# Kernel tuning notes

Hardware: AMD Instinct MI355X
Metric: run time of the kernel (lower is better)

## Reference

```python
import jax, jax.numpy as jnp
import numpy as np

DIM = 1536
HEADS = 12
HD = DIM // HEADS           # 128
C = HD // 2                 # 64 rotary pairs per head
B = 1
F_, H_, W_ = 16, 16, 16
S = F_ * H_ * W_            # 4096
MAXPOS = 1024
EPS = 1e-6
SPLITS = (C - 2 * (C // 3), C // 3, C // 3)  # (22, 21, 21)


def setup_inputs() -> dict:
    key = jax.random.key(0)
    ks = jax.random.split(key, 8)
    std = 0.02
    x = jax.random.normal(ks[0], (B, S, DIM), jnp.float32)
    seq_lens = jnp.full((B,), S, dtype=jnp.int32)
    grid_sizes = jnp.tile(jnp.array([[F_, H_, W_]], jnp.int32), (B, 1))
    # rotary angle table: per split, theta_j = pos / 10000^(j/size)
    angs = []
    pos = jnp.arange(MAXPOS, dtype=jnp.float32)
    for sz in SPLITS:
        inv = 1.0 / (10000.0 ** (jnp.arange(sz, dtype=jnp.float32) / sz))
        angs.append(jnp.outer(pos, inv))
    freqs = jnp.concatenate(angs, axis=1)  # [MAXPOS, C]
    return {
        "x": x,
        "seq_lens": seq_lens,
        "grid_sizes": grid_sizes,
        "freqs": freqs,
        "wq": jax.random.normal(ks[1], (DIM, DIM), jnp.float32) * std,
        "bq": jnp.zeros((DIM,), jnp.float32),
        "wk": jax.random.normal(ks[2], (DIM, DIM), jnp.float32) * std,
        "bk": jnp.zeros((DIM,), jnp.float32),
        "wv": jax.random.normal(ks[3], (DIM, DIM), jnp.float32) * std,
        "bv": jnp.zeros((DIM,), jnp.float32),
        "wo": jax.random.normal(ks[4], (DIM, DIM), jnp.float32) * std,
        "bo": jnp.zeros((DIM,), jnp.float32),
        "gq": jnp.ones((DIM,), jnp.float32),
        "gk": jnp.ones((DIM,), jnp.float32),
    }


def _rms_norm(x, g):
    # x * rsqrt(mean(x^2) + eps) * g  (WanRMSNorm)
    var = jnp.mean(jnp.square(x), axis=-1, keepdims=True)
    return x * jax.lax.rsqrt(var + EPS) * g


def _rope(x, freqs, f, h, w):
    # x: [b, s, n, hd]; freqs: [MAXPOS, C] angles; grid (f,h,w), s = f*h*w
    fa = freqs[:f, : SPLITS[0]]
    ha = freqs[:h, SPLITS[0] : SPLITS[0] + SPLITS[1]]
    wa = freqs[:w, SPLITS[0] + SPLITS[1] :]
    ang = jnp.concatenate(
        [
            jnp.broadcast_to(fa[:, None, None, :], (f, h, w, SPLITS[0])),
            jnp.broadcast_to(ha[None, :, None, :], (f, h, w, SPLITS[1])),
            jnp.broadcast_to(wa[None, None, :, :], (f, h, w, SPLITS[2])),
        ],
        axis=-1,
    ).reshape(f * h * w, 1, C)  # [s, 1, C] broadcasts over heads
    cos, sin = jnp.cos(ang), jnp.sin(ang)
    xr = x[..., 0::2]  # real parts of complex pairs
    xi = x[..., 1::2]  # imag parts
    out_r = xr * cos - xi * sin
    out_i = xr * sin + xi * cos
    return jnp.stack([out_r, out_i], axis=-1).reshape(x.shape)


def reference(x, seq_lens, grid_sizes, freqs, wq, bq, wk, bk, wv, bv, wo, bo, gq, gk):
    b, s = x.shape[:2]
    q = _rms_norm(x @ wq.T + bq, gq).reshape(b, s, HEADS, HD)
    k = _rms_norm(x @ wk.T + bk, gk).reshape(b, s, HEADS, HD)
    v = (x @ wv.T + bv).reshape(b, s, HEADS, HD)
    # all samples share the same grid (static for jit)
    q = _rope(q, freqs, F_, H_, W_)
    k = _rope(k, freqs, F_, H_, W_)
    scale = 1.0 / np.sqrt(HD)
    scores = jnp.einsum("bqnd,bknd->bnqk", q, k) * scale  # [b, n, s, s]
    k_pos = jnp.arange(s)
    mask = k_pos[None, None, None, :] < seq_lens[:, None, None, None]
    scores = scores + jnp.where(mask, 0.0, -1e9)
    attn = jax.nn.softmax(scores, axis=-1)
    out = jnp.einsum("bnqk,bknd->bqnd", attn, v).reshape(b, s, DIM)
    return out @ wo.T + bo
```

## Files before the change

kernel.cpp:

```cpp
#include <hip/hip_runtime.h>
#include <hip/hip_bf16.h>

#define DIM   1536
#define HEADS 12
#define HD    128
#define SEQ   4096
#define QSCALE 0.08838834764831845f
#define LOG2E 1.44269504088896f

typedef __attribute__((ext_vector_type(8))) short short8;
typedef __attribute__((ext_vector_type(4))) float f32x4;
typedef __attribute__((ext_vector_type(16))) float f32x16;

__device__ __forceinline__ unsigned short f2bf(float f) {
    __hip_bfloat16 h = __float2bfloat16(f);
    return *reinterpret_cast<unsigned short*>(&h);
}
__device__ __forceinline__ float bf2f(unsigned short u) {
    return __uint_as_float(((unsigned int)u) << 16);
}
__device__ __forceinline__ void async_cp16(void* lds, const void* g) {
    __builtin_amdgcn_global_load_lds(
        (const __attribute__((address_space(1))) unsigned int*)g,
        (__attribute__((address_space(3))) unsigned int*)lds, 16, 0, 0);
}

__global__ __launch_bounds__(256) void gemm_qkv(
    const float* __restrict__ x,
    const float* __restrict__ wq, const float* __restrict__ bq,
    const float* __restrict__ wk, const float* __restrict__ bk,
    const float* __restrict__ wv, const float* __restrict__ bv,
    __hip_bfloat16* __restrict__ yq, __hip_bfloat16* __restrict__ yk,
    __hip_bfloat16* __restrict__ vrow)
{
    __shared__ __align__(16) short As[128][40];
    __shared__ __align__(16) short Bs[128][40];
    const int z  = blockIdx.z;
    const float* W    = (z == 0) ? wq : (z == 1) ? wk : wv;
    const float* bias = (z == 0) ? bq : (z == 1) ? bk : bv;
    __hip_bfloat16* outp = (z == 0) ? yq : (z == 1) ? yk : vrow;
    const int bm0 = blockIdx.x * 128;
    const int bn0 = blockIdx.y * 128;
    const int tid  = threadIdx.x;
    const int lane = tid & 63;
    const int wid  = tid >> 6;
    const int wm = (wid >> 1) * 64;
    const int wn = (wid & 1)  * 64;
    const int fr = lane & 15;
    const int fc = (lane >> 4) * 8;
    const int srow = tid >> 3;
    const int scol = (tid & 7) * 4;

    f32x4 acc[4][4] = {};

    for (int kt = 0; kt < DIM; kt += 32) {
        #pragma unroll
        for (int p = 0; p < 4; ++p) {
            const int r = srow + p * 32;
            float4 va = *reinterpret_cast<const float4*>(&x[(size_t)(bm0 + r) * DIM + kt + scol]);
            float4 vb = *reinterpret_cast<const float4*>(&W[(size_t)(bn0 + r) * DIM + kt + scol]);
            uint2 pa, pb;
            pa.x = (unsigned int)f2bf(va.x) | ((unsigned int)f2bf(va.y) << 16);
            pa.y = (unsigned int)f2bf(va.z) | ((unsigned int)f2bf(va.w) << 16);
            pb.x = (unsigned int)f2bf(vb.x) | ((unsigned int)f2bf(vb.y) << 16);
            pb.y = (unsigned int)f2bf(vb.z) | ((unsigned int)f2bf(vb.w) << 16);
            *reinterpret_cast<uint2*>(&As[r][scol]) = pa;
            *reinterpret_cast<uint2*>(&Bs[r][scol]) = pb;
        }
        __syncthreads();
        short8 af[4], bf8[4];
        #pragma unroll
        for (int m = 0; m < 4; m++) af[m]  = *reinterpret_cast<const short8*>(&As[wm + m * 16 + fr][fc]);
        #pragma unroll
        for (int n = 0; n < 4; n++) bf8[n] = *reinterpret_cast<const short8*>(&Bs[wn + n * 16 + fr][fc]);
        #pragma unroll
        for (int m = 0; m < 4; m++)
            #pragma unroll
            for (int n = 0; n < 4; n++)
                acc[m][n] = __builtin_amdgcn_mfma_f32_16x16x32_bf16(af[m], bf8[n], acc[m][n], 0, 0, 0);
        __syncthreads();
    }

    const int crow0 = bm0 + wm + (lane >> 4) * 4;
    const int ccol0 = bn0 + wn + fr;
    #pragma unroll
    for (int n = 0; n < 4; n++) {
        const int col = ccol0 + n * 16;
        const float bb = bias[col];
        #pragma unroll
        for (int m = 0; m < 4; m++)
            #pragma unroll
            for (int r = 0; r < 4; r++)
                outp[(size_t)(crow0 + m * 16 + r) * DIM + col] =
                    __float2bfloat16(acc[m][n][r] + bb);
    }
}

__global__ __launch_bounds__(256) void rmsnorm_rope(
    __hip_bfloat16* __restrict__ yq, __hip_bfloat16* __restrict__ yk,
    const float* __restrict__ gq, const float* __restrict__ gk,
    const float* __restrict__ freqs)
{
    const int s = blockIdx.x;
    const int z = blockIdx.y;
    __hip_bfloat16* y = z ? yk : yq;
    const float* g = z ? gk : gq;
    const int t = threadIdx.x;

    float xr[3], xi[3];
    float ss = 0.f;
    #pragma unroll
    for (int i = 0; i < 3; i++) {
        const int p = t + i * 256;
        const unsigned int uu = *reinterpret_cast<const unsigned int*>(&y[(size_t)s * DIM + 2 * p]);
        xr[i] = bf2f((unsigned short)(uu & 0xffffu));
        xi[i] = bf2f((unsigned short)(uu >> 16));
        ss += xr[i] * xr[i] + xi[i] * xi[i];
    }
    #pragma unroll
    for (int m = 1; m < 64; m <<= 1) ss += __shfl_xor(ss, m, 64);
    __shared__ float red[4];
    if ((t & 63) == 0) red[t >> 6] = ss;
    __syncthreads();
    const float sum = red[0] + red[1] + red[2] + red[3];
    const float rs = rsqrtf(sum * (1.0f / DIM) + 1e-6f);
    const int f = s >> 8, hh = (s >> 4) & 15, ww = s & 15;
    const float osc = z ? 1.0f : QSCALE;
    #pragma unroll
    for (int i = 0; i < 3; i++) {
        const int p = t + i * 256;
        const int cc = p & 63;
        const int pos = (cc < 22) ? f : (cc < 43) ? hh : ww;
        const float ang = freqs[pos * 64 + cc];
        float sn, cs;
        sincosf(ang, &sn, &cs);
        const float a = xr[i] * rs * g[2 * p];
        const float b = xi[i] * rs * g[2 * p + 1];
        const unsigned int pk = (unsigned int)f2bf((a * cs - b * sn) * osc)
                              | ((unsigned int)f2bf((a * sn + b * cs) * osc) << 16);
        *reinterpret_cast<unsigned int*>(&y[(size_t)s * DIM + 2 * p]) = pk;
    }
}

__global__ __launch_bounds__(256) void transpose_v(
    const __hip_bfloat16* __restrict__ vrow,
    __hip_bfloat16* __restrict__ vT)
{
    __shared__ __align__(16) short tile[64][72];
    const int s0 = blockIdx.x * 64;
    const int c0 = blockIdx.y * 64;
    const int t = threadIdx.x;
    #pragma unroll
    for (int i = 0; i < 2; i++) {
        const int ch = t + i * 256;
        const int r = ch >> 3, cc = (ch & 7) * 8;
        *reinterpret_cast<int4*>(&tile[r][cc]) =
            *reinterpret_cast<const int4*>(&vrow[(size_t)(s0 + r) * DIM + c0 + cc]);
    }
    __syncthreads();
    #pragma unroll
    for (int i = 0; i < 2; i++) {
        const int ch = t + i * 256;
        const int c = ch & 63, sc = (ch >> 6) * 8;
        unsigned int w0 = (unsigned short)tile[sc + 0][c] | ((unsigned int)(unsigned short)tile[sc + 1][c] << 16);
        unsigned int w1 = (unsigned short)tile[sc + 2][c] | ((unsigned int)(unsigned short)tile[sc + 3][c] << 16);
        unsigned int w2 = (unsigned short)tile[sc + 4][c] | ((unsigned int)(unsigned short)tile[sc + 5][c] << 16);
        unsigned int w3 = (unsigned short)tile[sc + 6][c] | ((unsigned int)(unsigned short)tile[sc + 7][c] << 16);
        int4 val;
        val.x = (int)w0; val.y = (int)w1; val.z = (int)w2; val.w = (int)w3;
        *reinterpret_cast<int4*>(&vT[(size_t)(c0 + c) * SEQ + s0 + sc]) = val;
    }
}

__global__ __launch_bounds__(256, 2) void flash_attn(
    const __hip_bfloat16* __restrict__ qb,
    const __hip_bfloat16* __restrict__ kb,
    const __hip_bfloat16* __restrict__ vT,
    const int* __restrict__ seq_lens,
    __hip_bfloat16* __restrict__ attno)
{
    __shared__ __align__(16) short Ks[2][64][128];
    __shared__ __align__(16) short Vs[2][128][64];
    const int qt = blockIdx.x;
    const int h  = blockIdx.y;
    const int tid = threadIdx.x;
    const int lane = tid & 63;
    const int w = tid >> 6;
    const int q5 = lane & 31;
    const int hi = lane >> 5;
    const int seqlen = seq_lens[0];
    const int swz = (lane & 7) << 4;

    short8 qf[8];
    const int qrow = qt * 128 + w * 32 + q5;
    #pragma unroll
    for (int s = 0; s < 8; s++)
        qf[s] = *reinterpret_cast<const short8*>(&qb[(size_t)qrow * DIM + h * HD + s * 16 + hi * 8]);

    f32x16 oacc[4] = {};
    float m = -1e30f, l = 0.f;

    const int kROW = w * 4 + (lane >> 4);
    const int kCOL = ((lane & 15) ^ (kROW & 7)) * 8;
    const int vROW = w * 8 + (lane >> 3);
    const int vCOL = (((lane & 7) ^ (vROW & 7))) * 8;

    #pragma unroll
    for (int i = 0; i < 4; i++) {
        async_cp16(&Ks[0][i * 16 + w * 4][0],
                   kb + (size_t)(i * 16 + kROW) * DIM + h * HD + kCOL);
        async_cp16(&Vs[0][i * 32 + w * 8][0],
                   vT + ((size_t)h * HD + i * 32 + vROW) * SEQ + vCOL);
    }
    __syncthreads();

    for (int t = 0; t < SEQ / 64; t++) {
        const int cur = t & 1;
        const int kbase = t * 64;
        if (t + 1 < SEQ / 64) {
            const int nb = kbase + 64;
            #pragma unroll
            for (int i = 0; i < 4; i++) {
                async_cp16(&Ks[cur ^ 1][i * 16 + w * 4][0],
                           kb + (size_t)(nb + i * 16 + kROW) * DIM + h * HD + kCOL);
                async_cp16(&Vs[cur ^ 1][i * 32 + w * 8][0],
                           vT + ((size_t)h * HD + i * 32 + vROW) * SEQ + nb + vCOL);
            }
        }
        const char* Kp = (const char*)&Ks[cur][0][0];
        const char* Vp = (const char*)&Vs[cur][0][0];

        f32x16 sacc[2] = {};
        __builtin_amdgcn_s_setprio(1);
        #pragma unroll
        for (int s = 0; s < 8; s++) {
            #pragma unroll
            for (int kbk = 0; kbk < 2; kbk++) {
                short8 kf = *reinterpret_cast<const short8*>(
                    Kp + (kbk * 32 + q5) * 256 + ((s * 32 + hi * 16) ^ swz));
                sacc[kbk] = __builtin_amdgcn_mfma_f32_32x32x16_bf16(kf, qf[s], sacc[kbk], 0, 0, 0);
            }
        }
        __builtin_amdgcn_s_setprio(0);

        float tmax = -1e30f;
        if (kbase + 64 <= seqlen) {
            #pragma unroll
            for (int kbk = 0; kbk < 2; kbk++)
                #pragma unroll
                for (int r = 0; r < 16; r++) tmax = fmaxf(tmax, sacc[kbk][r]);
        } else {
            #pragma unroll
            for (int kbk = 0; kbk < 2; kbk++) {
                #pragma unroll
                for (int r = 0; r < 16; r++) {
                    const int key = kbase + kbk * 32 + (r & 3) + 8 * (r >> 2) + 4 * hi;
                    const float sv = (key < seqlen) ? sacc[kbk][r] : -1e30f;
                    sacc[kbk][r] = sv;
                    tmax = fmaxf(tmax, sv);
                }
            }
        }
        tmax = fmaxf(tmax, __shfl_xor(tmax, 32, 64));

        if (!__all(tmax <= m + 8.0f)) {
            const float mn = fmaxf(m, tmax);
            const float alpha = exp2f((m - mn) * LOG2E);
            m = mn;
            l *= alpha;
            #pragma unroll
            for (int cb = 0; cb < 4; cb++)
                #pragma unroll
                for (int r = 0; r < 16; r++) oacc[cb][r] *= alpha;
        }

        float ps = 0.f;
        #pragma unroll
        for (int kbk = 0; kbk < 2; kbk++) {
            #pragma unroll
            for (int r = 0; r < 16; r++) {
                const float p = exp2f((sacc[kbk][r] - m) * LOG2E);
                sacc[kbk][r] = p;
                ps += p;
            }
        }
        ps += __shfl_xor(ps, 32, 64);
        l += ps;

        unsigned int W[2][4][2];
        #pragma unroll
        for (int kbk = 0; kbk < 2; kbk++)
            #pragma unroll
            for (int tq = 0; tq < 4; tq++) {
                W[kbk][tq][0] = (unsigned int)f2bf(sacc[kbk][4 * tq + 0])
                              | ((unsigned int)f2bf(sacc[kbk][4 * tq + 1]) << 16);
                W[kbk][tq][1] = (unsigned int)f2bf(sacc[kbk][4 * tq + 2])
                              | ((unsigned int)f2bf(sacc[kbk][4 * tq + 3]) << 16);
            }

        #pragma unroll
        for (int ks = 0; ks < 4; ks++) {
            const int kbk = ks >> 1;
            const int te = (ks & 1) * 2, to = te + 1;
            const int a0 = (int)W[kbk][te][0], a1 = (int)W[kbk][te][1];
            const int b0 = (int)W[kbk][to][0], b1 = (int)W[kbk][to][1];
            const int xa0 = __shfl_xor(a0, 32, 64);
            const int xa1 = __shfl_xor(a1, 32, 64);
            const int xb0 = __shfl_xor(b0, 32, 64);
            const int xb1 = __shfl_xor(b1, 32, 64);
            int4 pwv;
            pwv.x = hi ? xb0 : a0;
            pwv.y = hi ? xb1 : a1;
            pwv.z = hi ? b0  : xa0;
            pwv.w = hi ? b1  : xa1;
            const short8 pf = __builtin_bit_cast(short8, pwv);
            __builtin_amdgcn_s_setprio(1);
            #pragma unroll
            for (int cb = 0; cb < 4; cb++) {
                short8 vf = *reinterpret_cast<const short8*>(
                    Vp + (cb * 32 + q5) * 128 + ((ks * 32 + hi * 16) ^ swz));
                oacc[cb] = __builtin_amdgcn_mfma_f32_32x32x16_bf16(vf, pf, oacc[cb], 0, 0, 0);
            }
            __builtin_amdgcn_s_setprio(0);
        }
        __syncthreads();
    }

    const float inv_l = 1.f / l;
    const size_t obase = (size_t)qrow * DIM + h * HD;
    #pragma unroll
    for (int cb = 0; cb < 4; cb++) {
        #pragma unroll
        for (int tq = 0; tq < 4; tq++) {
            uint2 pko;
            pko.x = (unsigned int)f2bf(oacc[cb][4 * tq + 0] * inv_l)
                  | ((unsigned int)f2bf(oacc[cb][4 * tq + 1] * inv_l) << 16);
            pko.y = (unsigned int)f2bf(oacc[cb][4 * tq + 2] * inv_l)
                  | ((unsigned int)f2bf(oacc[cb][4 * tq + 3] * inv_l) << 16);
            *reinterpret_cast<uint2*>(&attno[obase + cb * 32 + 8 * tq + 4 * hi]) = pko;
        }
    }
}

__global__ __launch_bounds__(256) void gemm_out(
    const __hip_bfloat16* __restrict__ A,
    const float* __restrict__ W,
    const float* __restrict__ bias,
    float* __restrict__ outp)
{
    __shared__ __align__(16) short As[128][40];
    __shared__ __align__(16) short Bs[128][40];
    const int bm0 = blockIdx.x * 128;
    const int bn0 = blockIdx.y * 128;
    const int tid = threadIdx.x;
    const int lane = tid & 63;
    const int wid = tid >> 6;
    const int wm = (wid >> 1) * 64;
    const int wn = (wid & 1) * 64;
    const int fr = lane & 15;
    const int fc = (lane >> 4) * 8;
    const int srow = tid >> 3;
    const int scol = (tid & 7) * 4;

    f32x4 acc[4][4] = {};

    for (int kt = 0; kt < DIM; kt += 32) {
        #pragma unroll
        for (int i = 0; i < 2; i++) {
            const int ch = tid + i * 256;
            const int r = ch >> 2, cc = (ch & 3) * 8;
            *reinterpret_cast<int4*>(&As[r][cc]) =
                *reinterpret_cast<const int4*>(&A[(size_t)(bm0 + r) * DIM + kt + cc]);
        }
        #pragma unroll
        for (int p = 0; p < 4; p++) {
            const int r = srow + p * 32;
            float4 vb = *reinterpret_cast<const float4*>(&W[(size_t)(bn0 + r) * DIM + kt + scol]);
            uint2 pb;
            pb.x = (unsigned int)f2bf(vb.x) | ((unsigned int)f2bf(vb.y) << 16);
            pb.y = (unsigned int)f2bf(vb.z) | ((unsigned int)f2bf(vb.w) << 16);
            *reinterpret_cast<uint2*>(&Bs[r][scol]) = pb;
        }
        __syncthreads();
        short8 af[4], bf8[4];
        #pragma unroll
        for (int m = 0; m < 4; m++) af[m]  = *reinterpret_cast<const short8*>(&As[wm + m * 16 + fr][fc]);
        #pragma unroll
        for (int n = 0; n < 4; n++) bf8[n] = *reinterpret_cast<const short8*>(&Bs[wn + n * 16 + fr][fc]);
        #pragma unroll
        for (int m = 0; m < 4; m++)
            #pragma unroll
            for (int n = 0; n < 4; n++)
                acc[m][n] = __builtin_amdgcn_mfma_f32_16x16x32_bf16(af[m], bf8[n], acc[m][n], 0, 0, 0);
        __syncthreads();
    }

    const int crow0 = bm0 + wm + (lane >> 4) * 4;
    const int ccol0 = bn0 + wn + fr;
    #pragma unroll
    for (int n = 0; n < 4; n++) {
        const int col = ccol0 + n * 16;
        const float bb = bias[col];
        #pragma unroll
        for (int m = 0; m < 4; m++)
            #pragma unroll
            for (int r = 0; r < 4; r++)
                outp[(size_t)(crow0 + m * 16 + r) * DIM + col] = acc[m][n][r] + bb;
    }
}

extern "C" void kernel_launch(void* const* d_in, const int* in_sizes, int n_in,
                              void* d_out, int out_size, void* d_ws, size_t ws_size,
                              hipStream_t stream)
{
    const float* x        = (const float*)d_in[0];
    const int*   seq_lens = (const int*)d_in[1];
    const float* freqs    = (const float*)d_in[3];
    const float* wq = (const float*)d_in[4];
    const float* bq = (const float*)d_in[5];
    const float* wk = (const float*)d_in[6];
    const float* bk = (const float*)d_in[7];
    const float* wv = (const float*)d_in[8];
    const float* bv = (const float*)d_in[9];
    const float* wo = (const float*)d_in[10];
    const float* bo = (const float*)d_in[11];
    const float* gq = (const float*)d_in[12];
    const float* gk = (const float*)d_in[13];
    float* out = (float*)d_out;

    char* ws = (char*)d_ws;
    __hip_bfloat16* yq    = (__hip_bfloat16*)(ws);
    __hip_bfloat16* yk    = (__hip_bfloat16*)(ws + 12582912);
    __hip_bfloat16* vrow  = (__hip_bfloat16*)(ws + 25165824);
    __hip_bfloat16* vT    = (__hip_bfloat16*)(ws + 37748736);
    __hip_bfloat16* attno = (__hip_bfloat16*)(ws + 25165824);

    dim3 blk(256);
    gemm_qkv    <<<dim3(32, 12, 3), blk, 0, stream>>>(x, wq, bq, wk, bk, wv, bv, yq, yk, vrow);
    rmsnorm_rope<<<dim3(4096, 2),   blk, 0, stream>>>(yq, yk, gq, gk, freqs);
    transpose_v <<<dim3(64, 24),    blk, 0, stream>>>(vrow, vT);
    flash_attn  <<<dim3(32, 12),    blk, 0, stream>>>(yq, yk, vT, seq_lens, attno);
    gemm_out    <<<dim3(32, 12),    blk, 0, stream>>>(attno, wo, bo, out);
}
```

Baseline: 403.5 us.

## Pre-convert inputs and weights to bf16 and use async global-to-LDS loads in GEMMs

Adds a conversion kernel that casts x and the four weight matrices to bf16 in workspace (and temporarily in the output buffer) before the GEMMs. The QKV and output GEMMs then stage tiles with direct global-to-LDS 16-byte copies instead of loading fp32, converting in registers and storing to LDS. This halves the bytes the GEMMs read and removes conversion work from their inner loops. In exchange it adds five extra launches and an extra pass over the fp32 data, and it drops the LDS row padding, which may cause bank conflicts on fragment reads.

```diff
diff --git a/kernel.cpp b/kernel.cpp
--- a/kernel.cpp
+++ b/kernel.cpp
@@ -25,18 +25,33 @@
         (__attribute__((address_space(3))) unsigned int*)lds, 16, 0, 0);
 }
 
+__global__ __launch_bounds__(256) void convert_bf16(
+    const float* __restrict__ src, __hip_bfloat16* __restrict__ dst, int n8)
+{
+    const int i = blockIdx.x * 256 + threadIdx.x;
+    if (i >= n8) return;
+    const float4 a = *reinterpret_cast<const float4*>(src + (size_t)i * 8);
+    const float4 b = *reinterpret_cast<const float4*>(src + (size_t)i * 8 + 4);
+    uint4 o;
+    o.x = (unsigned int)f2bf(a.x) | ((unsigned int)f2bf(a.y) << 16);
+    o.y = (unsigned int)f2bf(a.z) | ((unsigned int)f2bf(a.w) << 16);
+    o.z = (unsigned int)f2bf(b.x) | ((unsigned int)f2bf(b.y) << 16);
+    o.w = (unsigned int)f2bf(b.z) | ((unsigned int)f2bf(b.w) << 16);
+    *reinterpret_cast<uint4*>(dst + (size_t)i * 8) = o;
+}
+
 __global__ __launch_bounds__(256) void gemm_qkv(
-    const float* __restrict__ x,
-    const float* __restrict__ wq, const float* __restrict__ bq,
-    const float* __restrict__ wk, const float* __restrict__ bk,
-    const float* __restrict__ wv, const float* __restrict__ bv,
+    const __hip_bfloat16* __restrict__ xb,
+    const __hip_bfloat16* __restrict__ wqb, const float* __restrict__ bq,
+    const __hip_bfloat16* __restrict__ wkb, const float* __restrict__ bk,
+    const __hip_bfloat16* __restrict__ wvb, const float* __restrict__ bv,
     __hip_bfloat16* __restrict__ yq, __hip_bfloat16* __restrict__ yk,
     __hip_bfloat16* __restrict__ vrow)
 {
-    __shared__ __align__(16) short As[128][40];
-    __shared__ __align__(16) short Bs[128][40];
+    __shared__ __align__(16) short As[128][32];
+    __shared__ __align__(16) short Bs[128][32];
     const int z  = blockIdx.z;
-    const float* W    = (z == 0) ? wq : (z == 1) ? wk : wv;
+    const __hip_bfloat16* W = (z == 0) ? wqb : (z == 1) ? wkb : wvb;
     const float* bias = (z == 0) ? bq : (z == 1) ? bk : bv;
     __hip_bfloat16* outp = (z == 0) ? yq : (z == 1) ? yk : vrow;
     const int bm0 = blockIdx.x * 128;
@@ -48,24 +63,18 @@
     const int wn = (wid & 1)  * 64;
     const int fr = lane & 15;
     const int fc = (lane >> 4) * 8;
-    const int srow = tid >> 3;
-    const int scol = (tid & 7) * 4;
+    const int srow = tid >> 2;
+    const int scol = (tid & 3) * 8;
 
     f32x4 acc[4][4] = {};
 
     for (int kt = 0; kt < DIM; kt += 32) {
         #pragma unroll
-        for (int p = 0; p < 4; ++p) {
-            const int r = srow + p * 32;
-            float4 va = *reinterpret_cast<const float4*>(&x[(size_t)(bm0 + r) * DIM + kt + scol]);
-            float4 vb = *reinterpret_cast<const float4*>(&W[(size_t)(bn0 + r) * DIM + kt + scol]);
-            uint2 pa, pb;
-            pa.x = (unsigned int)f2bf(va.x) | ((unsigned int)f2bf(va.y) << 16);
-            pa.y = (unsigned int)f2bf(va.z) | ((unsigned int)f2bf(va.w) << 16);
-            pb.x = (unsigned int)f2bf(vb.x) | ((unsigned int)f2bf(vb.y) << 16);
-            pb.y = (unsigned int)f2bf(vb.z) | ((unsigned int)f2bf(vb.w) << 16);
-            *reinterpret_cast<uint2*>(&As[r][scol]) = pa;
-            *reinterpret_cast<uint2*>(&Bs[r][scol]) = pb;
+        for (int i = 0; i < 2; i++) {
+            async_cp16(&As[i * 64 + ((tid >> 6) << 4)][0],
+                       xb + (size_t)(bm0 + i * 64 + srow) * DIM + kt + scol);
+            async_cp16(&Bs[i * 64 + ((tid >> 6) << 4)][0],
+                       W + (size_t)(bn0 + i * 64 + srow) * DIM + kt + scol);
         }
         __syncthreads();
         short8 af[4], bf8[4];
@@ -344,12 +353,12 @@
 
 __global__ __launch_bounds__(256) void gemm_out(
     const __hip_bfloat16* __restrict__ A,
-    const float* __restrict__ W,
+    const __hip_bfloat16* __restrict__ W,
     const float* __restrict__ bias,
     float* __restrict__ outp)
 {
-    __shared__ __align__(16) short As[128][40];
-    __shared__ __align__(16) short Bs[128][40];
+    __shared__ __align__(16) short As[128][32];
+    __shared__ __align__(16) short Bs[128][32];
     const int bm0 = blockIdx.x * 128;
     const int bn0 = blockIdx.y * 128;
     const int tid = threadIdx.x;
@@ -359,27 +368,18 @@
     const int wn = (wid & 1) * 64;
     const int fr = lane & 15;
     const int fc = (lane >> 4) * 8;
-    const int srow = tid >> 3;
-    const int scol = (tid & 7) * 4;
+    const int srow = tid >> 2;
+    const int scol = (tid & 3) * 8;
 
     f32x4 acc[4][4] = {};
 
     for (int kt = 0; kt < DIM; kt += 32) {
         #pragma unroll
         for (int i = 0; i < 2; i++) {
-            const int ch = tid + i * 256;
-            const int r = ch >> 2, cc = (ch & 3) * 8;
-            *reinterpret_cast<int4*>(&As[r][cc]) =
-                *reinterpret_cast<const int4*>(&A[(size_t)(bm0 + r) * DIM + kt + cc]);
-        }
-        #pragma unroll
-        for (int p = 0; p < 4; p++) {
-            const int r = srow + p * 32;
-            float4 vb = *reinterpret_cast<const float4*>(&W[(size_t)(bn0 + r) * DIM + kt + scol]);
-            uint2 pb;
-            pb.x = (unsigned int)f2bf(vb.x) | ((unsigned int)f2bf(vb.y) << 16);
-            pb.y = (unsigned int)f2bf(vb.z) | ((unsigned int)f2bf(vb.w) << 16);
-            *reinterpret_cast<uint2*>(&Bs[r][scol]) = pb;
+            async_cp16(&As[i * 64 + ((tid >> 6) << 4)][0],
+                       A + (size_t)(bm0 + i * 64 + srow) * DIM + kt + scol);
+            async_cp16(&Bs[i * 64 + ((tid >> 6) << 4)][0],
+                       W + (size_t)(bn0 + i * 64 + srow) * DIM + kt + scol);
         }
         __syncthreads();
         short8 af[4], bf8[4];
@@ -434,11 +434,21 @@
     __hip_bfloat16* vrow  = (__hip_bfloat16*)(ws + 25165824);
     __hip_bfloat16* vT    = (__hip_bfloat16*)(ws + 37748736);
     __hip_bfloat16* attno = (__hip_bfloat16*)(ws + 25165824);
+    __hip_bfloat16* xb    = (__hip_bfloat16*)(ws + 37748736);
+    __hip_bfloat16* wob   = (__hip_bfloat16*)(ws);
+    __hip_bfloat16* wqb   = (__hip_bfloat16*)d_out;
+    __hip_bfloat16* wkb   = wqb + 2359296;
+    __hip_bfloat16* wvb   = wkb + 2359296;
 
     dim3 blk(256);
-    gemm_qkv    <<<dim3(32, 12, 3), blk, 0, stream>>>(x, wq, bq, wk, bk, wv, bv, yq, yk, vrow);
+    convert_bf16<<<dim3(3072), blk, 0, stream>>>(x,  xb,  786432);
+    convert_bf16<<<dim3(1152), blk, 0, stream>>>(wq, wqb, 294912);
+    convert_bf16<<<dim3(1152), blk, 0, stream>>>(wk, wkb, 294912);
+    convert_bf16<<<dim3(1152), blk, 0, stream>>>(wv, wvb, 294912);
+    gemm_qkv    <<<dim3(32, 12, 3), blk, 0, stream>>>(xb, wqb, bq, wkb, bk, wvb, bv, yq, yk, vrow);
     rmsnorm_rope<<<dim3(4096, 2),   blk, 0, stream>>>(yq, yk, gq, gk, freqs);
     transpose_v <<<dim3(64, 24),    blk, 0, stream>>>(vrow, vT);
     flash_attn  <<<dim3(32, 12),    blk, 0, stream>>>(yq, yk, vT, seq_lens, attno);
-    gemm_out    <<<dim3(32, 12),    blk, 0, stream>>>(attno, wo, bo, out);
-}
+    convert_bf16<<<dim3(1152), blk, 0, stream>>>(wo, wob, 294912);
+    gemm_out    <<<dim3(32, 12),    blk, 0, stream>>>(attno, wob, bo, out);
+}
```

New measurement: 358.7 us. -11.1%, faster.
